# Performance work log

Hardware: AMD Instinct MI355X
Metric: run time of the kernel (lower is better)

The kernel has to match this reference:

```python
import jax, jax.numpy as jnp
import numpy as np

N_HEADS = 12
EPS = 1e-6
H_DIM = 768


def setup_inputs() -> dict:
    key = jax.random.key(0)
    ks = jax.random.split(key, 10)
    B, M, T, C = 2, 64, 512, H_DIM
    x = jax.random.normal(ks[0], (B, M, T, C), dtype=jnp.float32)
    mask = jnp.ones((B, M, T), dtype=jnp.float32)
    s = 1.0 / np.sqrt(C)
    Wq = jax.random.normal(ks[1], (C, C), dtype=jnp.float32) * s
    bq = jax.random.normal(ks[2], (C,), dtype=jnp.float32) * 0.01
    Wk = jax.random.normal(ks[3], (C, C), dtype=jnp.float32) * s
    bk = jax.random.normal(ks[4], (C,), dtype=jnp.float32) * 0.01
    Wv = jax.random.normal(ks[5], (C, C), dtype=jnp.float32) * s
    bv = jax.random.normal(ks[6], (C,), dtype=jnp.float32) * 0.01
    Wp = jax.random.normal(ks[7], (C, C), dtype=jnp.float32) * s
    bp = jax.random.normal(ks[8], (C,), dtype=jnp.float32) * 0.01
    return {"x": x, "mask": mask, "Wq": Wq, "bq": bq, "Wk": Wk, "bk": bk,
            "Wv": Wv, "bv": bv, "Wp": Wp, "bp": bp}


def reference(x, mask, Wq, bq, Wk, bk, Wv, bv, Wp, bp):
    B, M, T, C = x.shape
    N, D = N_HEADS, C // N_HEADS
    # projections: nn.Linear -> x @ W.T + b, then [B,M,T,N,D] -> [B,M,N,T,D]
    q = (x @ Wq.T + bq).reshape(B, M, T, N, D).transpose(0, 1, 3, 2, 4)
    k = (x @ Wk.T + bk).reshape(B, M, T, N, D).transpose(0, 1, 3, 2, 4)
    v = (x @ Wv.T + bv).reshape(B, M, T, N, D).transpose(0, 1, 3, 2, 4)
    q = jax.nn.elu(q) + 1.0
    k = jax.nn.elu(k) + 1.0
    k = k * mask[:, :, None, :, None]
    # KtV[b,m,n,d,e] = sum_t k[b,m,n,t,d] * v[b,m,n,t,e]   (small [D,D] per head)
    KtV = jnp.einsum('bmntd,bmnte->bmnde', k, v)
    # Z[b,m,n,t] = 1 / (q . sum_t' k + eps)
    Z = 1.0 / (jnp.einsum('bmntd,bmnd->bmnt', q, k.sum(axis=-2)) + EPS)
    # torch code does Z.expand(...,T,D) @ KtV, which equals Z * KtV.sum(over d)
    S = KtV.sum(axis=-2)                       # [B,M,N,E]
    V = Z[..., None] * S[:, :, :, None, :]     # [B,M,N,T,E]
    V = V.transpose(0, 1, 3, 2, 4).reshape(B, M, T, N * D)
    out = V @ Wp.T + bp
    return out
```

## Files before the change

kernel.cpp:

```cpp
#include <hip/hip_runtime.h>
#include <hip/hip_bf16.h>
#include <stdint.h>

typedef short short8 __attribute__((ext_vector_type(8)));
typedef float f32x4 __attribute__((ext_vector_type(4)));

#define EPS_Z 1e-6f

__device__ __forceinline__ unsigned short f2bf(float f) {
  uint32_t b = __float_as_uint(f);
  b += 0x7FFFu + ((b >> 16) & 1u);
  return (unsigned short)(b >> 16);
}
__device__ __forceinline__ float bf2f(unsigned short u) {
  return __uint_as_float(((uint32_t)u) << 16);
}

__device__ __forceinline__ void gl16(const unsigned short* g, unsigned short* l) {
  __builtin_amdgcn_global_load_lds(
      (const __attribute__((address_space(1))) unsigned int*)g,
      (__attribute__((address_space(3))) unsigned int*)l, 16, 0, 0);
}

__global__ __launch_bounds__(256) void k_cvt_all(
    const float* __restrict__ x, const float* __restrict__ Wk,
    const float* __restrict__ Wq, unsigned short* __restrict__ xbf,
    unsigned short* __restrict__ Wkbf, unsigned short* __restrict__ Wqbf) {
  const int bid = blockIdx.x;
  const float* in;
  unsigned short* out;
  int base;
  if (bid < 24576)      { in = x;  out = xbf;  base = bid; }
  else if (bid < 24864) { in = Wk; out = Wkbf; base = bid - 24576; }
  else                  { in = Wq; out = Wqbf; base = bid - 24864; }
  const int i = (base * 256 + threadIdx.x) * 8;
  float4 a = *(const float4*)(in + i);
  float4 b = *(const float4*)(in + i + 4);
  union { unsigned short u[8]; short8 v; } r;
  r.u[0] = f2bf(a.x); r.u[1] = f2bf(a.y); r.u[2] = f2bf(a.z); r.u[3] = f2bf(a.w);
  r.u[4] = f2bf(b.x); r.u[5] = f2bf(b.y); r.u[6] = f2bf(b.z); r.u[7] = f2bf(b.w);
  *(short8*)(out + i) = r.v;
}

__global__ __launch_bounds__(512, 2) void k_projqk(
    const unsigned short* __restrict__ xbf,
    const unsigned short* __restrict__ Wkbf,
    const unsigned short* __restrict__ Wqbf,
    const float* __restrict__ bk,
    const float* __restrict__ bq,
    const float* __restrict__ mask,
    float* __restrict__ kd,
    float* __restrict__ ksum_part,
    unsigned short* __restrict__ qbf)
{
  __shared__ unsigned short Ab[128][64];
  __shared__ unsigned short Bkb[128][64];
  __shared__ unsigned short Bqb[128][64];
  __shared__ float rowf[128];
  __shared__ float kcol[2][128];

  const int tid = threadIdx.x;
  const int lane = tid & 63;
  const int wid = tid >> 6;
  const int isQ = wid >> 2;
  const int w2 = wid & 3;
  const int wr = w2 >> 1, wc = w2 & 1;
  const int colTile = blockIdx.x;
  const int rowTile = blockIdx.y;
  const int bm = rowTile >> 2;
  const int trow = rowTile & 3;
  const size_t rowBase = (size_t)rowTile * 128;
  const int colBase = colTile * 128;
  const int lrow = lane & 15;
  const int lgrp = lane >> 4;

  if (tid < 128) rowf[tid] = mask[bm * 512 + trow * 128 + tid];

  f32x4 acc[4][4] = {};

  for (int kt = 0; kt < 12; ++kt) {
    const int k0 = kt * 64;
    __syncthreads();
#pragma unroll
    for (int c = 0; c < 2; ++c) {
      const int chunk = c * 512 + tid;
      const int r = chunk >> 3;
      const int cc = chunk & 7;
      const int scc = cc ^ (r & 7);
      const int ldst = c * 4096 + wid * 512;
      gl16(xbf + (rowBase + r) * 768 + k0 + scc * 8, &Ab[0][0] + ldst);
      gl16(Wkbf + (size_t)(colBase + r) * 768 + k0 + scc * 8, &Bkb[0][0] + ldst);
      gl16(Wqbf + (size_t)(colBase + r) * 768 + k0 + scc * 8, &Bqb[0][0] + ldst);
    }
    __syncthreads();
    const unsigned short* Bsel = isQ ? &Bqb[0][0] : &Bkb[0][0];
#pragma unroll
    for (int kk = 0; kk < 64; kk += 32) {
      short8 av[4], bv4[4];
#pragma unroll
      for (int rf = 0; rf < 4; ++rf) {
        const int row = wr * 64 + rf * 16 + lrow;
        const int cidx = ((kk >> 3) + lgrp) ^ (row & 7);
        av[rf] = *(const short8*)&Ab[row][cidx * 8];
      }
#pragma unroll
      for (int cf = 0; cf < 4; ++cf) {
        const int row = wc * 64 + cf * 16 + lrow;
        const int cidx = ((kk >> 3) + lgrp) ^ (row & 7);
        bv4[cf] = *(const short8*)(Bsel + row * 64 + cidx * 8);
      }
#pragma unroll
      for (int rf = 0; rf < 4; ++rf)
#pragma unroll
        for (int cf = 0; cf < 4; ++cf)
          acc[rf][cf] = __builtin_amdgcn_mfma_f32_16x16x32_bf16(
              av[rf], bv4[cf], acc[rf][cf], 0, 0, 0);
    }
  }

  const float* bias = isQ ? bq : bk;
  float bvv[4];
#pragma unroll
  for (int cf = 0; cf < 4; ++cf)
    bvv[cf] = bias[colBase + wc * 64 + cf * 16 + lrow];
#pragma unroll
  for (int rf = 0; rf < 4; ++rf)
#pragma unroll
    for (int cf = 0; cf < 4; ++cf)
#pragma unroll
      for (int j = 0; j < 4; ++j) {
        float v = acc[rf][cf][j] + bvv[cf];
        v = (v > 0.0f) ? (v + 1.0f) : __expf(v);
        if (!isQ) v *= rowf[wr * 64 + rf * 16 + lgrp * 4 + j];
        acc[rf][cf][j] = v;
      }

  const int head = colTile * 2 + wc;

  if (!isQ) {
#pragma unroll
    for (int rf = 0; rf < 4; ++rf)
#pragma unroll
      for (int j = 0; j < 4; ++j) {
        float s = acc[rf][0][j] + acc[rf][1][j] + acc[rf][2][j] + acc[rf][3][j];
        s += __shfl_xor(s, 1, 64);
        s += __shfl_xor(s, 2, 64);
        s += __shfl_xor(s, 4, 64);
        s += __shfl_xor(s, 8, 64);
        if ((lane & 15) == 0) {
          const int t = trow * 128 + wr * 64 + rf * 16 + lgrp * 4 + j;
          kd[((size_t)bm * 512 + t) * 12 + head] = s;
        }
      }
#pragma unroll
    for (int cf = 0; cf < 4; ++cf) {
      float s = 0.f;
#pragma unroll
      for (int rf = 0; rf < 4; ++rf)
#pragma unroll
        for (int j = 0; j < 4; ++j) s += acc[rf][cf][j];
      s += __shfl_xor(s, 16, 64);
      s += __shfl_xor(s, 32, 64);
      if (lane < 16) kcol[wr][wc * 64 + cf * 16 + lane] = s;
    }
  } else {
#pragma unroll
    for (int rf = 0; rf < 4; ++rf)
#pragma unroll
      for (int j = 0; j < 4; ++j) {
        const int t = trow * 128 + wr * 64 + rf * 16 + lgrp * 4 + j;
        unsigned short* qp = qbf + (((size_t)bm * 12 + head) * 512 + t) * 64 + lrow;
#pragma unroll
        for (int cf = 0; cf < 4; ++cf)
          qp[cf * 16] = f2bf(acc[rf][cf][j]);
      }
  }

  __syncthreads();
  if (tid < 128)
    ksum_part[((size_t)bm * 4 + trow) * 768 + colBase + tid] =
        kcol[0][tid] + kcol[1][tid];
}

__global__ __launch_bounds__(256) void k_xkz(const unsigned short* __restrict__ xbf,
                                             const float* __restrict__ kd,
                                             float* __restrict__ xk_part,
                                             const unsigned short* __restrict__ qbf,
                                             const float* __restrict__ ksum_part,
                                             float* __restrict__ Z) {
  const int bid = blockIdx.x, tid = threadIdx.x;
  if (bid < 512) {
    __shared__ float kdl[128][12];
    const int bm = bid >> 2, ts = bid & 3;
    for (int i = tid; i < 128 * 12; i += 256)
      kdl[i / 12][i % 12] = kd[((size_t)bm * 512 + ts * 128 + i / 12) * 12 + (i % 12)];
    __syncthreads();
    if (tid < 192) {
      float a[12][4];
#pragma unroll
      for (int n = 0; n < 12; ++n)
#pragma unroll
        for (int j = 0; j < 4; ++j) a[n][j] = 0.f;
      const int c = tid * 4;
      const unsigned short* xp = xbf + ((size_t)bm * 512 + ts * 128) * 768 + c;
      for (int t = 0; t < 128; ++t) {
        ushort4 xv = *(const ushort4*)(xp + (size_t)t * 768);
        const float x0 = bf2f(xv.x), x1 = bf2f(xv.y), x2 = bf2f(xv.z), x3 = bf2f(xv.w);
#pragma unroll
        for (int n = 0; n < 12; ++n) {
          const float kv = kdl[t][n];
          a[n][0] += kv * x0; a[n][1] += kv * x1; a[n][2] += kv * x2; a[n][3] += kv * x3;
        }
      }
      float* op = xk_part + ((size_t)bm * 4 + ts) * 12 * 768 + c;
#pragma unroll
      for (int n = 0; n < 12; ++n)
        *(float4*)(op + (size_t)n * 768) = make_float4(a[n][0], a[n][1], a[n][2], a[n][3]);
    }
  } else {
    __shared__ float ksum_l[768];
    const int b2 = bid - 512;
    const int bm = b2 >> 2, ts = b2 & 3;
    for (int i = tid; i < 768; i += 256) {
      const float* kp = ksum_part + (size_t)bm * 3072 + i;
      ksum_l[i] = kp[0] + kp[768] + kp[1536] + kp[2304];
    }
    __syncthreads();
#pragma unroll
    for (int i = 0; i < 6; ++i) {
      const int task = i * 256 + tid;
      const int n = task >> 7;
      const int t = ts * 128 + (task & 127);
      const unsigned short* qp = qbf + (((size_t)bm * 12 + n) * 512 + t) * 64;
      const float* kp = &ksum_l[n * 64];
      float s = 0.f;
#pragma unroll
      for (int c = 0; c < 8; ++c) {
        short8 qv = *(const short8*)(qp + c * 8);
        s += bf2f((unsigned short)qv[0]) * kp[c * 8 + 0]
           + bf2f((unsigned short)qv[1]) * kp[c * 8 + 1]
           + bf2f((unsigned short)qv[2]) * kp[c * 8 + 2]
           + bf2f((unsigned short)qv[3]) * kp[c * 8 + 3]
           + bf2f((unsigned short)qv[4]) * kp[c * 8 + 4]
           + bf2f((unsigned short)qv[5]) * kp[c * 8 + 5]
           + bf2f((unsigned short)qv[6]) * kp[c * 8 + 6]
           + bf2f((unsigned short)qv[7]) * kp[c * 8 + 7];
      }
      Z[((size_t)bm * 12 + n) * 512 + t] = 1.0f / (s + EPS_Z);
    }
  }
}

__global__ __launch_bounds__(256) void k_sg(const float* __restrict__ ksum_part,
                                            const float* __restrict__ xk_part,
                                            const float* __restrict__ Wv,
                                            const float* __restrict__ bv,
                                            const float* __restrict__ Wp,
                                            float* __restrict__ G) {
  __shared__ __align__(16) float xk_l[2][768];
  __shared__ __align__(16) float S_l[2][64];
  __shared__ float kdsum_l[2];
  const int n = blockIdx.x, bm0 = blockIdx.y * 2, tid = threadIdx.x;

  for (int task = tid; task < 384; task += 256) {
    const int b = task / 192, c4 = task - b * 192;
    const float* xp = xk_part + (size_t)(bm0 + b) * 4 * 9216 + n * 768 + c4 * 4;
    float4 a = *(const float4*)(xp);
    float4 bb = *(const float4*)(xp + 9216);
    float4 c = *(const float4*)(xp + 18432);
    float4 d = *(const float4*)(xp + 27648);
    *(float4*)&xk_l[b][c4 * 4] = make_float4(a.x + bb.x + c.x + d.x,
                                             a.y + bb.y + c.y + d.y,
                                             a.z + bb.z + c.z + d.z,
                                             a.w + bb.w + c.w + d.w);
  }
  if (tid < 128) {
    const int b = tid >> 6, d = tid & 63;
    const float* kp = ksum_part + (size_t)(bm0 + b) * 3072 + n * 64 + d;
    float s = kp[0] + kp[768] + kp[1536] + kp[2304];
    s += __shfl_xor(s, 1, 64);
    s += __shfl_xor(s, 2, 64);
    s += __shfl_xor(s, 4, 64);
    s += __shfl_xor(s, 8, 64);
    s += __shfl_xor(s, 16, 64);
    s += __shfl_xor(s, 32, 64);
    if (d == 0) kdsum_l[b] = s;
  }
  __syncthreads();

  {
    const int e = tid >> 2, q = tid & 3;
    const float4* wv = (const float4*)(Wv + (size_t)(n * 64 + e) * 768 + q * 192);
    const float4* x0 = (const float4*)(&xk_l[0][0] + q * 192);
    const float4* x1 = (const float4*)(&xk_l[1][0] + q * 192);
    float s0 = 0.f, s1 = 0.f;
#pragma unroll
    for (int i = 0; i < 48; ++i) {
      float4 w = wv[i];
      float4 a = x0[i], b = x1[i];
      s0 += w.x * a.x + w.y * a.y + w.z * a.z + w.w * a.w;
      s1 += w.x * b.x + w.y * b.y + w.z * b.z + w.w * b.w;
    }
    s0 += __shfl_xor(s0, 1, 64);
    s0 += __shfl_xor(s0, 2, 64);
    s1 += __shfl_xor(s1, 1, 64);
    s1 += __shfl_xor(s1, 2, 64);
    if (q == 0) {
      const float bve = bv[n * 64 + e];
      S_l[0][e] = s0 + bve * kdsum_l[0];
      S_l[1][e] = s1 + bve * kdsum_l[1];
    }
  }
  __syncthreads();

#pragma unroll
  for (int r = 0; r < 3; ++r) {
    const int p = r * 256 + tid;
    const float4* wp = (const float4*)(Wp + (size_t)p * 768 + n * 64);
    const float4* s0p = (const float4*)&S_l[0][0];
    const float4* s1p = (const float4*)&S_l[1][0];
    float g0 = 0.f, g1 = 0.f;
#pragma unroll
    for (int i = 0; i < 16; ++i) {
      float4 w = wp[i];
      float4 a = s0p[i], b = s1p[i];
      g0 += w.x * a.x + w.y * a.y + w.z * a.z + w.w * a.w;
      g1 += w.x * b.x + w.y * b.y + w.z * b.z + w.w * b.w;
    }
    G[((size_t)(bm0 + 0) * 12 + n) * 768 + p] = g0;
    G[((size_t)(bm0 + 1) * 12 + n) * 768 + p] = g1;
  }
}

__global__ __launch_bounds__(256) void k_out(const float* __restrict__ Z,
                                             const float* __restrict__ G,
                                             const float* __restrict__ bp,
                                             float* __restrict__ outp) {
  __shared__ __align__(16) float G_l[9216];
  __shared__ float Z_l[768];
  __shared__ __align__(16) float bp_l[768];
  const int bm = blockIdx.x;
  const int tbase = blockIdx.y * 64;
  const int tid = threadIdx.x;
  for (int i = tid; i < 9216; i += 256) G_l[i] = G[(size_t)bm * 9216 + i];
  for (int i = tid; i < 768; i += 256) {
    bp_l[i] = bp[i];
    Z_l[i] = Z[((size_t)bm * 12 + (i >> 6)) * 512 + tbase + (i & 63)];
  }
  __syncthreads();
  for (int it = 0; it < 48; ++it) {
    const int idx = it * 1024 + tid * 4;
    const int t = idx / 768;
    const int p = idx - t * 768;
    float4 o = *(const float4*)&bp_l[p];
#pragma unroll
    for (int n = 0; n < 12; ++n) {
      const float z = Z_l[n * 64 + t];
      const float4 g = *(const float4*)&G_l[n * 768 + p];
      o.x += z * g.x; o.y += z * g.y; o.z += z * g.z; o.w += z * g.w;
    }
    *(float4*)&outp[((size_t)bm * 512 + tbase + t) * 768 + p] = o;
  }
}

extern "C" void kernel_launch(void* const* d_in, const int* in_sizes, int n_in,
                              void* d_out, int out_size, void* d_ws, size_t ws_size,
                              hipStream_t stream) {
  const float* x    = (const float*)d_in[0];
  const float* mask = (const float*)d_in[1];
  const float* Wq   = (const float*)d_in[2];
  const float* bq   = (const float*)d_in[3];
  const float* Wk   = (const float*)d_in[4];
  const float* bk   = (const float*)d_in[5];
  const float* Wv   = (const float*)d_in[6];
  const float* bv   = (const float*)d_in[7];
  const float* Wp   = (const float*)d_in[8];
  const float* bp   = (const float*)d_in[9];
  float* outp = (float*)d_out;

  char* ws = (char*)d_ws;
  unsigned short* xbf  = (unsigned short*)(ws);
  unsigned short* Wkbf = (unsigned short*)(ws + 100663296);
  unsigned short* Wqbf = (unsigned short*)(ws + 101842944);
  float* kd        = (float*)(ws + 103022592);
  float* ksum_part = (float*)(ws + 106168320);
  float* xk_part   = (float*)(ws + 107741184);
  float* Zb        = (float*)(ws + 126615552);
  float* G         = (float*)(ws + 129761280);
  unsigned short* qbf = (unsigned short*)d_out;

  hipLaunchKernelGGL(k_cvt_all, dim3(25152), dim3(256), 0, stream,
                     x, Wk, Wq, xbf, Wkbf, Wqbf);
  hipLaunchKernelGGL(k_projqk, dim3(6, 512), dim3(512), 0, stream,
                     xbf, Wkbf, Wqbf, bk, bq, mask, kd, ksum_part, qbf);
  hipLaunchKernelGGL(k_xkz, dim3(1024), dim3(256), 0, stream,
                     xbf, kd, xk_part, qbf, ksum_part, Zb);
  hipLaunchKernelGGL(k_sg, dim3(12, 64), dim3(256), 0, stream,
                     ksum_part, xk_part, Wv, bv, Wp, G);
  hipLaunchKernelGGL(k_out, dim3(128, 8), dim3(256), 0, stream, Zb, G, bp, outp);
}
```

Baseline: 429.0 us.

## Double-buffer QK projection LDS tiles with K-step 32 to overlap loads and MFMA

Replaces the single 64-wide K tile with two 32-wide LDS buffers per operand in the fused Q/K projection GEMM. The next slice is prefetched via global_load_lds while MFMAs run on the current one, which takes the load latency off the critical path. The cost is twice as many K iterations and barriers and a new XOR swizzle for 32-element rows. A staging bug here could corrupt data.

```diff
diff --git a/kernel.cpp b/kernel.cpp
--- a/kernel.cpp
+++ b/kernel.cpp
@@ -42,6 +42,44 @@
   *(short8*)(out + i) = r.v;
 }
 
+__device__ __forceinline__ void stage32(
+    const unsigned short* __restrict__ xbf,
+    const unsigned short* __restrict__ Wkbf,
+    const unsigned short* __restrict__ Wqbf,
+    size_t rowBase, int colBase, int k0, int tid,
+    unsigned short* A, unsigned short* K, unsigned short* Q) {
+  const int r = tid >> 2;
+  const int scc = (tid & 3) ^ ((r >> 1) & 3);
+  const int dst = tid * 8;
+  gl16(xbf + (rowBase + r) * 768 + k0 + scc * 8, A + dst);
+  gl16(Wkbf + (size_t)(colBase + r) * 768 + k0 + scc * 8, K + dst);
+  gl16(Wqbf + (size_t)(colBase + r) * 768 + k0 + scc * 8, Q + dst);
+}
+
+__device__ __forceinline__ void compute32(
+    const unsigned short* Abuf, const unsigned short* Bbuf,
+    int wr, int wc, int lrow, int lgrp, f32x4 (&acc)[4][4]) {
+  short8 av[4], bv4[4];
+#pragma unroll
+  for (int rf = 0; rf < 4; ++rf) {
+    const int row = wr * 64 + rf * 16 + lrow;
+    const int cidx = lgrp ^ ((row >> 1) & 3);
+    av[rf] = *(const short8*)(Abuf + row * 32 + cidx * 8);
+  }
+#pragma unroll
+  for (int cf = 0; cf < 4; ++cf) {
+    const int row = wc * 64 + cf * 16 + lrow;
+    const int cidx = lgrp ^ ((row >> 1) & 3);
+    bv4[cf] = *(const short8*)(Bbuf + row * 32 + cidx * 8);
+  }
+#pragma unroll
+  for (int rf = 0; rf < 4; ++rf)
+#pragma unroll
+    for (int cf = 0; cf < 4; ++cf)
+      acc[rf][cf] = __builtin_amdgcn_mfma_f32_16x16x32_bf16(
+          av[rf], bv4[cf], acc[rf][cf], 0, 0, 0);
+}
+
 __global__ __launch_bounds__(512, 2) void k_projqk(
     const unsigned short* __restrict__ xbf,
     const unsigned short* __restrict__ Wkbf,
@@ -53,9 +91,9 @@
     float* __restrict__ ksum_part,
     unsigned short* __restrict__ qbf)
 {
-  __shared__ unsigned short Ab[128][64];
-  __shared__ unsigned short Bkb[128][64];
-  __shared__ unsigned short Bqb[128][64];
+  __shared__ unsigned short Ab[2][128][32];
+  __shared__ unsigned short Bkb[2][128][32];
+  __shared__ unsigned short Bqb[2][128][32];
   __shared__ float rowf[128];
   __shared__ float kcol[2][128];
 
@@ -78,44 +116,22 @@
 
   f32x4 acc[4][4] = {};
 
-  for (int kt = 0; kt < 12; ++kt) {
-    const int k0 = kt * 64;
+  unsigned short* A0 = &Ab[0][0][0];  unsigned short* A1 = &Ab[1][0][0];
+  unsigned short* K0 = &Bkb[0][0][0]; unsigned short* K1 = &Bkb[1][0][0];
+  unsigned short* Q0 = &Bqb[0][0][0]; unsigned short* Q1 = &Bqb[1][0][0];
+
+  stage32(xbf, Wkbf, Wqbf, rowBase, colBase, 0, tid, A0, K0, Q0);
+  __syncthreads();
+
+#pragma unroll 1
+  for (int kt = 0; kt < 24; kt += 2) {
+    stage32(xbf, Wkbf, Wqbf, rowBase, colBase, (kt + 1) * 32, tid, A1, K1, Q1);
+    compute32(A0, isQ ? Q0 : K0, wr, wc, lrow, lgrp, acc);
     __syncthreads();
-#pragma unroll
-    for (int c = 0; c < 2; ++c) {
-      const int chunk = c * 512 + tid;
-      const int r = chunk >> 3;
-      const int cc = chunk & 7;
-      const int scc = cc ^ (r & 7);
-      const int ldst = c * 4096 + wid * 512;
-      gl16(xbf + (rowBase + r) * 768 + k0 + scc * 8, &Ab[0][0] + ldst);
-      gl16(Wkbf + (size_t)(colBase + r) * 768 + k0 + scc * 8, &Bkb[0][0] + ldst);
-      gl16(Wqbf + (size_t)(colBase + r) * 768 + k0 + scc * 8, &Bqb[0][0] + ldst);
-    }
+    if (kt + 2 < 24)
+      stage32(xbf, Wkbf, Wqbf, rowBase, colBase, (kt + 2) * 32, tid, A0, K0, Q0);
+    compute32(A1, isQ ? Q1 : K1, wr, wc, lrow, lgrp, acc);
     __syncthreads();
-    const unsigned short* Bsel = isQ ? &Bqb[0][0] : &Bkb[0][0];
-#pragma unroll
-    for (int kk = 0; kk < 64; kk += 32) {
-      short8 av[4], bv4[4];
-#pragma unroll
-      for (int rf = 0; rf < 4; ++rf) {
-        const int row = wr * 64 + rf * 16 + lrow;
-        const int cidx = ((kk >> 3) + lgrp) ^ (row & 7);
-        av[rf] = *(const short8*)&Ab[row][cidx * 8];
-      }
-#pragma unroll
-      for (int cf = 0; cf < 4; ++cf) {
-        const int row = wc * 64 + cf * 16 + lrow;
-        const int cidx = ((kk >> 3) + lgrp) ^ (row & 7);
-        bv4[cf] = *(const short8*)(Bsel + row * 64 + cidx * 8);
-      }
-#pragma unroll
-      for (int rf = 0; rf < 4; ++rf)
-#pragma unroll
-        for (int cf = 0; cf < 4; ++cf)
-          acc[rf][cf] = __builtin_amdgcn_mfma_f32_16x16x32_bf16(
-              av[rf], bv4[cf], acc[rf][cf], 0, 0, 0);
-    }
   }
 
   const float* bias = isQ ? bq : bk;
```

Result: no change. 433.5 us (+1.0%).
